# Performance work log

Measured on AMD Instinct MI355X. Metric: run time of the kernel, lower is better.

The kernel has to match this reference:

```python
import jax, jax.numpy as jnp
import numpy as np

NEG = -10000.0
START_TAG = 62
STOP_TAG = 63


def setup_inputs() -> dict:
    key = jax.random.key(0)
    k1, k2, k3 = jax.random.split(key, 3)
    S, B, T = 512, 512, 64
    feats = jax.random.normal(k1, (S, B, T), dtype=jnp.float32)
    tags = jax.random.randint(k2, (S, B), 0, START_TAG, dtype=jnp.int32)
    mask = jnp.ones((S, B), dtype=jnp.float32)
    # nn.Parameter(torch.randn(T,T)) with start row / stop col clamped to -1e4
    transitions = jax.random.normal(k3, (T, T), dtype=jnp.float32)
    transitions = transitions.at[START_TAG, :].set(NEG).at[:, STOP_TAG].set(NEG)
    return {"feats": feats, "tags": tags, "mask": mask, "transitions": transitions}


def _score_sentence(feats, tags, mask, transitions):
    # feats: [S,B,T], tags/mask: [S,B]
    S, B, T = feats.shape
    emission = jnp.take_along_axis(feats, tags[:, :, None], axis=2)[..., 0]  # [S,B]
    start = jnp.full((1, B), START_TAG, dtype=tags.dtype)
    tags_ext = jnp.concatenate([start, tags], axis=0)  # [S+1,B]
    trans = transitions[tags_ext[:-1], tags_ext[1:]]  # [S,B]
    score = jnp.sum((emission + trans) * mask, axis=0)  # [B]
    last_idx = mask.sum(axis=0).astype(jnp.int32) - 1  # [B]
    last_tags = tags[last_idx, jnp.arange(B)]
    return score + transitions[last_tags, STOP_TAG]


def _forward_alg(feats, mask, transitions):
    S, B, T = feats.shape
    log_alpha0 = jnp.full((B, T), NEG, dtype=feats.dtype).at[:, START_TAG].set(0.0)

    def step(log_alpha, xs):
        f_i, m_i = xs  # [B,T], [B]
        # broadcast: [B, prev_tag, next_tag]
        scores = log_alpha[:, :, None] + transitions[None, :, :] + f_i[:, None, :]
        nxt = jax.nn.logsumexp(scores, axis=1)  # [B,T]
        log_alpha = jnp.where(m_i[:, None] > 0, nxt, log_alpha)
        return log_alpha, None

    log_alpha, _ = jax.lax.scan(step, log_alpha0, (feats, mask))
    return jax.nn.logsumexp(log_alpha + transitions[STOP_TAG][None, :], axis=1)  # [B]


def reference(feats, tags, mask, transitions):
    score_true = _score_sentence(feats, tags, mask, transitions)
    log_z = _forward_alg(feats, mask, transitions)
    return jnp.mean(log_z - score_true)
```

## Files before the change

kernel.cpp:

```cpp
#include <hip/hip_runtime.h>

#define NEG (-10000.0f)
#define START_TAG 62
#define STOP_TAG 63
#define SLEN 512
#define BATCH 512
#define NTAG 64

typedef float f32x2 __attribute__((ext_vector_type(2)));
typedef float f32x4 __attribute__((ext_vector_type(4)));

__device__ __forceinline__ float readlane_f(float v, int lane) {
    return __uint_as_float(__builtin_amdgcn_readlane(__float_as_uint(v), lane));
}

__global__ __launch_bounds__(64) __attribute__((amdgpu_waves_per_eu(1, 1)))
void crf_fwd(const float* __restrict__ feats,
             const int* __restrict__ tags,
             const float* __restrict__ mask,
             const float* __restrict__ trans,
             float* __restrict__ diff ) {
    const int b = blockIdx.x;
    const int j = threadIdx.x;

    __shared__ float smask[SLEN];
    __shared__ __align__(16) float qraw[2][NTAG];

    f32x2 e2[32];
    float colsum = 0.0f;
#pragma unroll
    for (int r = 0; r < 32; ++r) {
        float lo = __expf(trans[(2 * r) * NTAG + j]);
        float hi = __expf(trans[(2 * r + 1) * NTAG + j]);
        e2[r] = (f32x2){lo, hi};
        colsum += lo + hi;
    }
    const float tstop = trans[STOP_TAG * NTAG + j];

    float mreg[8];
#pragma unroll
    for (int k = 0; k < 8; ++k) mreg[k] = mask[(64 * k + j) * BATCH + b];
#pragma unroll
    for (int k = 0; k < 8; ++k) smask[64 * k + j] = mreg[k];

    float f_s0 = feats[(0 * BATCH + b) * NTAG + j];
    float m0 = readlane_f(mreg[0], 0);
    float alpha0 = (m0 > 0.0f) ? (NEG + log1pf(colsum) + f_s0)
                               : ((j == START_TAG) ? 0.0f : NEG);
    const float C0 = readlane_f(alpha0, START_TAG);
    float q = __expf(alpha0 - C0);

    if (j == 0) smask[0] = 0.0f;
    qraw[0][j] = q;
    __syncthreads();

    const float* fp = feats + (size_t)b * NTAG + j;
    float fr[8];
#pragma unroll
    for (int t = 0; t < 8; ++t) fr[t] = fp[(size_t)t * BATCH * NTAG];

    float rinv = 1.0f;
    int kcur = 0;
    int ktot = 0;

    for (int blk = 0; blk < 64; ++blk) {
#pragma unroll
        for (int t = 0; t < 8; ++t) {
            const int s = blk * 8 + t;
            const int ph = t & 1;

            const float mk = smask[s];

            float ef = __expf(fr[t]);
            int sp = s + 8;
            if (sp > SLEN - 1) sp = SLEN - 1;
            fr[t] = fp[(size_t)sp * BATCH * NTAG];
            float efr = ef * rinv;

            const f32x4* qv = (const f32x4*)(&qraw[ph][0]);
            f32x2 acc[8];
#pragma unroll
            for (int c = 0; c < 8; ++c) acc[c] = (f32x2){0.0f, 0.0f};
#pragma unroll
            for (int r = 0; r < 16; ++r) {
                f32x4 q4 = qv[r];
                f32x2 qlo = (f32x2){q4.x, q4.y};
                f32x2 qhi = (f32x2){q4.z, q4.w};
                acc[(2 * r) & 7] = qlo * e2[2 * r] + acc[(2 * r) & 7];
                acc[(2 * r + 1) & 7] = qhi * e2[2 * r + 1] + acc[(2 * r + 1) & 7];
            }
            f32x2 s01 = (acc[0] + acc[1]) + (acc[2] + acc[3]);
            f32x2 s23 = (acc[4] + acc[5]) + (acc[6] + acc[7]);
            f32x2 sall = s01 + s23;
            float acc_s = sall.x + sall.y;

            float qn = acc_s * efr;
            bool upd = (mk > 0.0f);
            q = upd ? qn : q;
            qraw[ph ^ 1][j] = q;

            ktot = upd ? (ktot + kcur) : ktot;
            unsigned a0u = __builtin_amdgcn_readfirstlane(__float_as_uint(acc_s));
            int ke = (int)((a0u >> 23) & 0xffu) - 127;
            ke = (ke < -60) ? -60 : ((ke > 60) ? 60 : ke);
            float rnew = __uint_as_float((unsigned)(127 - ke) << 23);
            rinv = upd ? rnew : rinv;
            kcur = upd ? ke : kcur;
        }
    }

    float et = __expf(tstop);
    float pe = q * et;
#pragma unroll
    for (int w = 32; w >= 1; w >>= 1) pe += __shfl_xor(pe, w, 64);
    float logz = __logf(pe) + C0 + (float)ktot * 0.6931471805599453f;

    float psc = 0.0f, pms = 0.0f;
#pragma unroll
    for (int k = 0; k < 8; ++k) {
        int s = j + 64 * k;
        int tg = tags[s * BATCH + b];
        float mk = mreg[k];
        int tprev = (s == 0) ? START_TAG : tags[(s - 1) * BATCH + b];
        float em = feats[((size_t)s * BATCH + b) * NTAG + tg];
        psc = fmaf(em + trans[tprev * NTAG + tg], mk, psc);
        pms += mk;
    }
#pragma unroll
    for (int w = 32; w >= 1; w >>= 1) {
        psc += __shfl_xor(psc, w, 64);
        pms += __shfl_xor(pms, w, 64);
    }

    if (j == 0) {
        int last_idx = (int)(pms + 0.5f) - 1;
        int ltag = tags[last_idx * BATCH + b];
        float score = psc + trans[ltag * NTAG + STOP_TAG];
        diff[b] = logz - score;
    }
}

__global__ __launch_bounds__(512) void crf_reduce(const float* __restrict__ diff,
                                                  float* __restrict__ out) {
    __shared__ float sdata[8];
    int t = threadIdx.x;
    float val = diff[t];
#pragma unroll
    for (int w = 32; w >= 1; w >>= 1)
        val += __shfl_xor(val, w, 64);
    if ((t & 63) == 0) sdata[t >> 6] = val;
    __syncthreads();
    if (t == 0) {
        float ssum = 0.0f;
        for (int i = 0; i < 8; ++i) ssum += sdata[i];
        out[0] = ssum * (1.0f / (float)BATCH);
    }
}

extern "C" void kernel_launch(void* const* d_in, const int* in_sizes, int n_in,
                              void* d_out, int out_size, void* d_ws, size_t ws_size,
                              hipStream_t stream) {
    const float* feats = (const float*)d_in[0];
    const int* tags = (const int*)d_in[1];
    const float* mask = (const float*)d_in[2];
    const float* trans = (const float*)d_in[3];
    float* out = (float*)d_out;
    float* diff = (float*)d_ws;

    crf_fwd<<<BATCH, 64, 0, stream>>>(feats, tags, mask, trans, diff);
    crf_reduce<<<1, 512, 0, stream>>>(diff, out);
}
```

Before: 199.0 us.

## Prefetch next-step alpha into registers and fuse final reduction via atomic ticket

Each step's recurrence now reads the freshly written q vector and next mask from LDS right after the store, into a register array, so the next iteration's FMA chain starts without a dependent LDS load. The accumulator zero-init is folded into the first FMAs. The separate reduction kernel is replaced by a last-block-done atomic ticket inside the main kernel, with a memset of the counter before launch. This adds more register pressure and a threadfence/atomic per block.

```diff
diff --git a/kernel.cpp b/kernel.cpp
--- a/kernel.cpp
+++ b/kernel.cpp
@@ -19,11 +19,13 @@
              const int* __restrict__ tags,
              const float* __restrict__ mask,
              const float* __restrict__ trans,
-             float* __restrict__ diff ) {
+             float* __restrict__ diff ,
+             float* __restrict__ out,
+             unsigned* __restrict__ done) {
     const int b = blockIdx.x;
     const int j = threadIdx.x;
 
-    __shared__ float smask[SLEN];
+    __shared__ float smask[SLEN + 1];
     __shared__ __align__(16) float qraw[2][NTAG];
 
     f32x2 e2[32];
@@ -50,9 +52,14 @@
     const float C0 = readlane_f(alpha0, START_TAG);
     float q = __expf(alpha0 - C0);
 
-    if (j == 0) smask[0] = 0.0f;
+    if (j == 0) { smask[0] = 0.0f; smask[SLEN] = 0.0f; }
     qraw[0][j] = q;
     __syncthreads();
+
+    f32x4 Q[16];
+#pragma unroll
+    for (int r = 0; r < 16; ++r) Q[r] = ((const f32x4*)&qraw[0][0])[r];
+    float mk = smask[0];
 
     const float* fp = feats + (size_t)b * NTAG + j;
     float fr[8];
@@ -69,25 +76,25 @@
             const int s = blk * 8 + t;
             const int ph = t & 1;
 
-            const float mk = smask[s];
-
             float ef = __expf(fr[t]);
             int sp = s + 8;
             if (sp > SLEN - 1) sp = SLEN - 1;
             fr[t] = fp[(size_t)sp * BATCH * NTAG];
             float efr = ef * rinv;
 
-            const f32x4* qv = (const f32x4*)(&qraw[ph][0]);
             f32x2 acc[8];
 #pragma unroll
-            for (int c = 0; c < 8; ++c) acc[c] = (f32x2){0.0f, 0.0f};
-#pragma unroll
             for (int r = 0; r < 16; ++r) {
-                f32x4 q4 = qv[r];
-                f32x2 qlo = (f32x2){q4.x, q4.y};
-                f32x2 qhi = (f32x2){q4.z, q4.w};
-                acc[(2 * r) & 7] = qlo * e2[2 * r] + acc[(2 * r) & 7];
-                acc[(2 * r + 1) & 7] = qhi * e2[2 * r + 1] + acc[(2 * r + 1) & 7];
+                f32x2 qlo = (f32x2){Q[r].x, Q[r].y};
+                f32x2 qhi = (f32x2){Q[r].z, Q[r].w};
+                const int c0 = (2 * r) & 7, c1 = (2 * r + 1) & 7;
+                if (r < 4) {
+                    acc[c0] = qlo * e2[2 * r];
+                    acc[c1] = qhi * e2[2 * r + 1];
+                } else {
+                    acc[c0] = qlo * e2[2 * r] + acc[c0];
+                    acc[c1] = qhi * e2[2 * r + 1] + acc[c1];
+                }
             }
             f32x2 s01 = (acc[0] + acc[1]) + (acc[2] + acc[3]);
             f32x2 s23 = (acc[4] + acc[5]) + (acc[6] + acc[7]);
@@ -98,6 +105,11 @@
             bool upd = (mk > 0.0f);
             q = upd ? qn : q;
             qraw[ph ^ 1][j] = q;
+
+#pragma unroll
+            for (int r = 0; r < 16; ++r)
+                Q[r] = ((const f32x4*)&qraw[ph ^ 1][0])[r];
+            mk = smask[s + 1];
 
             ktot = upd ? (ktot + kcur) : ktot;
             unsigned a0u = __builtin_amdgcn_readfirstlane(__float_as_uint(acc_s));
@@ -120,11 +132,11 @@
     for (int k = 0; k < 8; ++k) {
         int s = j + 64 * k;
         int tg = tags[s * BATCH + b];
-        float mk = mreg[k];
+        float mkk = mreg[k];
         int tprev = (s == 0) ? START_TAG : tags[(s - 1) * BATCH + b];
         float em = feats[((size_t)s * BATCH + b) * NTAG + tg];
-        psc = fmaf(em + trans[tprev * NTAG + tg], mk, psc);
-        pms += mk;
+        psc = fmaf(em + trans[tprev * NTAG + tg], mkk, psc);
+        pms += mkk;
     }
 #pragma unroll
     for (int w = 32; w >= 1; w >>= 1) {
@@ -138,22 +150,22 @@
         float score = psc + trans[ltag * NTAG + STOP_TAG];
         diff[b] = logz - score;
     }
-}
 
-__global__ __launch_bounds__(512) void crf_reduce(const float* __restrict__ diff,
-                                                  float* __restrict__ out) {
-    __shared__ float sdata[8];
-    int t = threadIdx.x;
-    float val = diff[t];
+    __threadfence();
+    unsigned ticket = 0;
+    if (j == 0) ticket = atomicAdd(done, 1u);
+    ticket = __builtin_amdgcn_readfirstlane(ticket);
+    if (ticket == (unsigned)(gridDim.x - 1)) {
+        __threadfence();
+        float ssum = 0.0f;
 #pragma unroll
-    for (int w = 32; w >= 1; w >>= 1)
-        val += __shfl_xor(val, w, 64);
-    if ((t & 63) == 0) sdata[t >> 6] = val;
-    __syncthreads();
-    if (t == 0) {
-        float ssum = 0.0f;
-        for (int i = 0; i < 8; ++i) ssum += sdata[i];
-        out[0] = ssum * (1.0f / (float)BATCH);
+        for (int w = 0; w < 8; ++w) {
+            float val = diff[w * 64 + j];
+#pragma unroll
+            for (int x = 32; x >= 1; x >>= 1) val += __shfl_xor(val, x, 64);
+            ssum += val;
+        }
+        if (j == 0) out[0] = ssum * (1.0f / (float)BATCH);
     }
 }
 
@@ -166,7 +178,8 @@
     const float* trans = (const float*)d_in[3];
     float* out = (float*)d_out;
     float* diff = (float*)d_ws;
+    unsigned* done = (unsigned*)((char*)d_ws + 2048);
 
-    crf_fwd<<<BATCH, 64, 0, stream>>>(feats, tags, mask, trans, diff);
-    crf_reduce<<<1, 512, 0, stream>>>(diff, out);
+    hipMemsetAsync(done, 0, sizeof(unsigned), stream);
+    crf_fwd<<<BATCH, 64, 0, stream>>>(feats, tags, mask, trans, diff, out, done);
 }
```

Measured after the change: 226.2 us. 1.14x slower.

## Broadcast alpha via readlane instead of LDS double-buffer in CRF recurrence

Applied to the files above, without the earlier changes.

Each timestep's 64 alpha values are now broadcast across the wavefront with v_readlane into scalar registers, replacing the LDS ping-pong buffer and its 128-bit loads. The matvec becomes scalar-operand FMAs against per-lane exp(transitions), and the feats prefetch depth drops from 8 to 4. This removes LDS store/load latency and waitcnt on the serial critical path. In exchange it adds 64 readlane instructions per step, which serialize through the scalar pipe with read-after-write hazards, and gives up the packed f32x2 FMAs.

```diff
diff --git a/kernel.cpp b/kernel.cpp
--- a/kernel.cpp
+++ b/kernel.cpp
@@ -6,9 +6,6 @@
 #define SLEN 512
 #define BATCH 512
 #define NTAG 64
-
-typedef float f32x2 __attribute__((ext_vector_type(2)));
-typedef float f32x4 __attribute__((ext_vector_type(4)));
 
 __device__ __forceinline__ float readlane_f(float v, int lane) {
     return __uint_as_float(__builtin_amdgcn_readlane(__float_as_uint(v), lane));
@@ -24,16 +21,13 @@
     const int j = threadIdx.x;
 
     __shared__ float smask[SLEN];
-    __shared__ __align__(16) float qraw[2][NTAG];
 
-    f32x2 e2[32];
+    float e[NTAG];
     float colsum = 0.0f;
 #pragma unroll
-    for (int r = 0; r < 32; ++r) {
-        float lo = __expf(trans[(2 * r) * NTAG + j]);
-        float hi = __expf(trans[(2 * r + 1) * NTAG + j]);
-        e2[r] = (f32x2){lo, hi};
-        colsum += lo + hi;
+    for (int i = 0; i < NTAG; ++i) {
+        e[i] = __expf(trans[i * NTAG + j]);
+        colsum += e[i];
     }
     const float tstop = trans[STOP_TAG * NTAG + j];
 
@@ -43,7 +37,7 @@
 #pragma unroll
     for (int k = 0; k < 8; ++k) smask[64 * k + j] = mreg[k];
 
-    float f_s0 = feats[(0 * BATCH + b) * NTAG + j];
+    float f_s0 = feats[(size_t)b * NTAG + j];
     float m0 = readlane_f(mreg[0], 0);
     float alpha0 = (m0 > 0.0f) ? (NEG + log1pf(colsum) + f_s0)
                                : ((j == START_TAG) ? 0.0f : NEG);
@@ -51,53 +45,48 @@
     float q = __expf(alpha0 - C0);
 
     if (j == 0) smask[0] = 0.0f;
-    qraw[0][j] = q;
     __syncthreads();
 
     const float* fp = feats + (size_t)b * NTAG + j;
-    float fr[8];
+    float fr[4];
 #pragma unroll
-    for (int t = 0; t < 8; ++t) fr[t] = fp[(size_t)t * BATCH * NTAG];
+    for (int t = 0; t < 4; ++t) fr[t] = fp[(size_t)t * BATCH * NTAG];
 
     float rinv = 1.0f;
     int kcur = 0;
     int ktot = 0;
 
-    for (int blk = 0; blk < 64; ++blk) {
+    for (int blk = 0; blk < 128; ++blk) {
 #pragma unroll
-        for (int t = 0; t < 8; ++t) {
-            const int s = blk * 8 + t;
-            const int ph = t & 1;
+        for (int t = 0; t < 4; ++t) {
+            const int s = blk * 4 + t;
 
             const float mk = smask[s];
 
             float ef = __expf(fr[t]);
-            int sp = s + 8;
+            int sp = s + 4;
             if (sp > SLEN - 1) sp = SLEN - 1;
             fr[t] = fp[(size_t)sp * BATCH * NTAG];
             float efr = ef * rinv;
 
-            const f32x4* qv = (const f32x4*)(&qraw[ph][0]);
-            f32x2 acc[8];
+            unsigned qu = __float_as_uint(q);
+            float su[64];
+            float acc[4] = {0.0f, 0.0f, 0.0f, 0.0f};
 #pragma unroll
-            for (int c = 0; c < 8; ++c) acc[c] = (f32x2){0.0f, 0.0f};
+            for (int i = 0; i < 8; ++i)
+                su[i] = __uint_as_float(__builtin_amdgcn_readlane(qu, i));
 #pragma unroll
-            for (int r = 0; r < 16; ++r) {
-                f32x4 q4 = qv[r];
-                f32x2 qlo = (f32x2){q4.x, q4.y};
-                f32x2 qhi = (f32x2){q4.z, q4.w};
-                acc[(2 * r) & 7] = qlo * e2[2 * r] + acc[(2 * r) & 7];
-                acc[(2 * r + 1) & 7] = qhi * e2[2 * r + 1] + acc[(2 * r + 1) & 7];
+            for (int i = 0; i < NTAG; ++i) {
+                if (i < NTAG - 8)
+                    su[i + 8] = __uint_as_float(
+                        __builtin_amdgcn_readlane(qu, i + 8));
+                acc[i & 3] = fmaf(su[i], e[i], acc[i & 3]);
             }
-            f32x2 s01 = (acc[0] + acc[1]) + (acc[2] + acc[3]);
-            f32x2 s23 = (acc[4] + acc[5]) + (acc[6] + acc[7]);
-            f32x2 sall = s01 + s23;
-            float acc_s = sall.x + sall.y;
+            float acc_s = (acc[0] + acc[1]) + (acc[2] + acc[3]);
 
             float qn = acc_s * efr;
             bool upd = (mk > 0.0f);
             q = upd ? qn : q;
-            qraw[ph ^ 1][j] = q;
 
             ktot = upd ? (ktot + kcur) : ktot;
             unsigned a0u = __builtin_amdgcn_readfirstlane(__float_as_uint(acc_s));
@@ -120,11 +109,11 @@
     for (int k = 0; k < 8; ++k) {
         int s = j + 64 * k;
         int tg = tags[s * BATCH + b];
-        float mk = mreg[k];
+        float mkk = mreg[k];
         int tprev = (s == 0) ? START_TAG : tags[(s - 1) * BATCH + b];
         float em = feats[((size_t)s * BATCH + b) * NTAG + tg];
-        psc = fmaf(em + trans[tprev * NTAG + tg], mk, psc);
-        pms += mk;
+        psc = fmaf(em + trans[tprev * NTAG + tg], mkk, psc);
+        pms += mkk;
     }
 #pragma unroll
     for (int w = 32; w >= 1; w >>= 1) {
```

Measured after the change: 232.9 us. +17.1%, slower.
